# Kernel optimization log

Measured on AMD Instinct MI355X. Metric: run time of the kernel, lower is better.

## Reference

```python
import math
import jax, jax.numpy as jnp
import numpy as np

jax.config.update("jax_enable_x64", True)  # original module computes attention in float64

MIN_NORM = 1e-08
B, S, G = 2, 2048, 16
D_MODEL, NHEAD = 512, 8
KDIM, VDIM = 512, 512
EK, EV = KDIM // NHEAD, VDIM // NHEAD
PARAM_SCALE = 0.02  # keep exp() in range; torch.randn params at this width would overflow exp


def setup_inputs() -> dict:
    key = jax.random.key(0)
    ks = jax.random.split(key, 9)
    f32 = jnp.float32
    return {
        "query": jax.random.normal(ks[0], (B, S, D_MODEL), f32),
        "key": jax.random.normal(ks[1], (B, S, D_MODEL), f32),
        "value": jax.random.normal(ks[2], (B, S, D_MODEL), f32),
        "context": jax.random.normal(ks[3], (B, G, D_MODEL), f32),
        "query_proj": jax.random.normal(ks[4], (1, D_MODEL, KDIM), f32) * PARAM_SCALE,
        "key_proj": jax.random.normal(ks[5], (1, D_MODEL, KDIM), f32) * PARAM_SCALE,
        "value_proj": jax.random.normal(ks[6], (1, D_MODEL, VDIM), f32) * PARAM_SCALE,
        "output_proj": jax.random.normal(ks[7], (1, VDIM, D_MODEL), f32) * PARAM_SCALE,
        "context_proj": jax.random.normal(ks[8], (1, D_MODEL, KDIM), f32) * PARAM_SCALE,
    }


def _causal_attention(queries, keys, values_list):
    # queries: (B,H,G,Ek) context heads; keys: (B,H,S,Ek); values: (B,H,S,Ev)
    q = queries.astype(jnp.float64)
    k = keys.astype(jnp.float64)
    d = k.shape[-1]
    w = jnp.einsum("bhge,bhse->bhgs", q, k) / math.sqrt(d)
    w = jnp.exp(w - jnp.mean(w))            # global mean, as in original
    norms = jnp.cumsum(w, axis=-1)          # (B,H,G,S)
    norms = jnp.where(norms <= MIN_NORM, MIN_NORM, norms)
    out = []
    for v in values_list:
        v = v.astype(jnp.float64)
        # (B,H,G,S,Ev) broadcast outer product, then causal prefix-sum over S
        wv = w[..., None] * v[..., None, :, :]
        rm = jnp.cumsum(wv, axis=-2) / norms[..., None]
        out.append(jnp.swapaxes(rm, -3, -2).astype(jnp.float32))  # (B,H,S,G,Ev)
    return out


def _forward(query, key, value, context, query_proj, key_proj, value_proj, output_proj, context_proj):
    Bb, L, E = query.shape
    Gg = context.shape[1]
    H, Ek, Ev = NHEAD, KDIM // NHEAD, VDIM // NHEAD
    cs = jnp.swapaxes((context @ context_proj).reshape(Bb, Gg, H, Ek), 1, 2)  # (B,H,G,Ek)
    qs = jnp.swapaxes((query @ query_proj).reshape(Bb, L, H, Ek), 1, 2)      # (B,H,S,Ek)
    kk = jnp.swapaxes((key @ key_proj).reshape(Bb, L, H, Ek), 1, 2)          # (B,H,S,Ek)
    vs = jnp.swapaxes((value @ value_proj).reshape(Bb, L, H, Ev), 1, 2)      # (B,H,S,Ev)
    rvm, rkm = _causal_attention(cs, kk, [vs, kk])  # (B,H,S,G,Ev), (B,H,S,G,Ek)
    weights = jnp.einsum("bhse,bhsge->bhsg", qs, rkm)
    weights = jax.nn.softmax(weights, axis=-1)
    out = jnp.einsum("bhsg,bhsge->bhse", weights, rvm)      # (B,H,S,Ev)
    out = jnp.swapaxes(out, 1, 2).reshape(Bb, L, H * Ev)    # (B,S,vdim)
    return out @ output_proj                                 # (B,S,d_model)


def reference(query, key, value, context, query_proj, key_proj, value_proj, output_proj, context_proj):
    return _forward(query, key, value, context, query_proj, key_proj, value_proj, output_proj, context_proj)
```

## Files before the change

### kernel.cpp

```cpp
#include <hip/hip_runtime.h>
#include <hip/hip_bf16.h>

#define BB 2
#define SS 2048
#define GG 16
#define HH 8
#define EE 64
#define DD 512
#define NCHUNK 32
#define CLEN 64
#define CS_STRIDE 132

typedef __attribute__((ext_vector_type(8))) short bf16x8;
typedef __attribute__((ext_vector_type(4))) float f32x4;

static __device__ __forceinline__ short f2bf(float x) {
  union { float f; unsigned u; } v; v.f = x;
  unsigned r = v.u + 0x7fffu + ((v.u >> 16) & 1u);
  return (short)(r >> 16);
}
static __device__ __forceinline__ float bf2f(short s) {
  return __uint_as_float(((unsigned)(unsigned short)s) << 16);
}
static __device__ __forceinline__ void bsplit(float x, short& hi, short& lo) {
  hi = f2bf(x);
  lo = f2bf(x - bf2f(hi));
}

__global__ __launch_bounds__(256) void cvtT4_bf16(const float* __restrict__ w0,
                                                  const float* __restrict__ w1,
                                                  const float* __restrict__ w2,
                                                  const float* __restrict__ w3,
                                                  short* __restrict__ o0,
                                                  short* __restrict__ o1,
                                                  short* __restrict__ o2,
                                                  short* __restrict__ o3) {
  const float* W; short* O;
  if (blockIdx.z == 0)      { W = w0; O = o0; }
  else if (blockIdx.z == 1) { W = w1; O = o1; }
  else if (blockIdx.z == 2) { W = w2; O = o2; }
  else                      { W = w3; O = o3; }
  __shared__ float t[32][33];
  const int tx = threadIdx.x, ty = threadIdx.y;
  const int k0 = blockIdx.x * 32, n0 = blockIdx.y * 32;
#pragma unroll
  for (int i = 0; i < 4; ++i)
    t[ty + i * 8][tx] = W[(size_t)(k0 + ty + i * 8) * DD + n0 + tx];
  __syncthreads();
#pragma unroll
  for (int i = 0; i < 4; ++i)
    O[(size_t)(n0 + ty + i * 8) * DD + k0 + tx] = f2bf(t[tx][ty + i * 8]);
}

#define LDA 72
__global__ __launch_bounds__(256) void proj_gemm(const float* __restrict__ a0,
                                                 const float* __restrict__ a1,
                                                 const float* __restrict__ a2,
                                                 const short* __restrict__ b0,
                                                 const short* __restrict__ b1,
                                                 const short* __restrict__ b2,
                                                 float* __restrict__ c0,
                                                 float* __restrict__ c1,
                                                 float* __restrict__ c2) {
  const float* A; const short* Bt; float* C;
  if (blockIdx.z == 0)      { A = a0; Bt = b0; C = c0; }
  else if (blockIdx.z == 1) { A = a1; Bt = b1; C = c1; }
  else                      { A = a2; Bt = b2; C = c2; }
  const int N = DD, K = DD;
  __shared__ short As[128 * LDA];
  __shared__ short Bs[64 * LDA];
  const int tid = threadIdx.x;
  const int m0 = blockIdx.y * 128, n0 = blockIdx.x * 64;
  const int wv = tid >> 6, lane = tid & 63;
  const int wm = wv * 32;
  const int r = lane & 15, q = lane >> 4;
  f32x4 acc[2][4] = {};
  for (int k0 = 0; k0 < K; k0 += 64) {
    float4 af[4][2];
    bf16x8 bvv[2];
#pragma unroll
    for (int it = 0; it < 4; ++it) {
      int idx = tid + it * 256;
      int row = idx >> 3, colq = (idx & 7) * 8;
      af[it][0] = *(const float4*)(A + (size_t)(m0 + row) * K + k0 + colq);
      af[it][1] = *(const float4*)(A + (size_t)(m0 + row) * K + k0 + colq + 4);
    }
#pragma unroll
    for (int it = 0; it < 2; ++it) {
      int idx = tid + it * 256;
      int row = idx >> 3, colq = (idx & 7) * 8;
      bvv[it] = *(const bf16x8*)(Bt + (size_t)(n0 + row) * K + k0 + colq);
    }
    __syncthreads();
#pragma unroll
    for (int it = 0; it < 4; ++it) {
      int idx = tid + it * 256;
      int row = idx >> 3, colq = (idx & 7) * 8;
      bf16x8 av;
      const float* p0 = (const float*)&af[it][0];
      const float* p1 = (const float*)&af[it][1];
      av[0] = f2bf(p0[0]); av[1] = f2bf(p0[1]); av[2] = f2bf(p0[2]); av[3] = f2bf(p0[3]);
      av[4] = f2bf(p1[0]); av[5] = f2bf(p1[1]); av[6] = f2bf(p1[2]); av[7] = f2bf(p1[3]);
      *(bf16x8*)(&As[row * LDA + colq]) = av;
    }
#pragma unroll
    for (int it = 0; it < 2; ++it) {
      int idx = tid + it * 256;
      int row = idx >> 3, colq = (idx & 7) * 8;
      *(bf16x8*)(&Bs[row * LDA + colq]) = bvv[it];
    }
    __syncthreads();
#pragma unroll
    for (int ks = 0; ks < 2; ++ks) {
      bf16x8 a0r = *(const bf16x8*)(&As[(wm + r) * LDA + ks * 32 + q * 8]);
      bf16x8 a1r = *(const bf16x8*)(&As[(wm + 16 + r) * LDA + ks * 32 + q * 8]);
#pragma unroll
      for (int j = 0; j < 4; ++j) {
        bf16x8 br = *(const bf16x8*)(&Bs[(j * 16 + r) * LDA + ks * 32 + q * 8]);
        acc[0][j] = __builtin_amdgcn_mfma_f32_16x16x32_bf16(a0r, br, acc[0][j], 0, 0, 0);
        acc[1][j] = __builtin_amdgcn_mfma_f32_16x16x32_bf16(a1r, br, acc[1][j], 0, 0, 0);
      }
    }
  }
#pragma unroll
  for (int i = 0; i < 2; ++i)
#pragma unroll
    for (int j = 0; j < 4; ++j)
#pragma unroll
      for (int reg = 0; reg < 4; ++reg) {
        int m = m0 + wm + i * 16 + q * 4 + reg;
        int n = n0 + j * 16 + r;
        C[(size_t)m * N + n] = acc[i][j][reg];
      }
}

__global__ __launch_bounds__(256) void gemm_bf16(const short* __restrict__ A,
                                                 const short* __restrict__ Bt,
                                                 float* __restrict__ C,
                                                 int M, int N, int K) {
  __shared__ short As[128 * LDA];
  __shared__ short Bs[64 * LDA];
  const int tid = threadIdx.x;
  const int m0 = blockIdx.y * 128, n0 = blockIdx.x * 64;
  const int wv = tid >> 6, lane = tid & 63;
  const int wm = wv * 32;
  const int r = lane & 15, q = lane >> 4;
  f32x4 acc[2][4] = {};
  for (int k0 = 0; k0 < K; k0 += 64) {
    bf16x8 av[4], bvv[2];
#pragma unroll
    for (int it = 0; it < 4; ++it) {
      int idx = tid + it * 256;
      int row = idx >> 3, colq = (idx & 7) * 8;
      av[it] = *(const bf16x8*)(A + (size_t)(m0 + row) * K + k0 + colq);
    }
#pragma unroll
    for (int it = 0; it < 2; ++it) {
      int idx = tid + it * 256;
      int row = idx >> 3, colq = (idx & 7) * 8;
      bvv[it] = *(const bf16x8*)(Bt + (size_t)(n0 + row) * K + k0 + colq);
    }
    __syncthreads();
#pragma unroll
    for (int it = 0; it < 4; ++it) {
      int idx = tid + it * 256;
      int row = idx >> 3, colq = (idx & 7) * 8;
      *(bf16x8*)(&As[row * LDA + colq]) = av[it];
    }
#pragma unroll
    for (int it = 0; it < 2; ++it) {
      int idx = tid + it * 256;
      int row = idx >> 3, colq = (idx & 7) * 8;
      *(bf16x8*)(&Bs[row * LDA + colq]) = bvv[it];
    }
    __syncthreads();
#pragma unroll
    for (int ks = 0; ks < 2; ++ks) {
      bf16x8 a0r = *(const bf16x8*)(&As[(wm + r) * LDA + ks * 32 + q * 8]);
      bf16x8 a1r = *(const bf16x8*)(&As[(wm + 16 + r) * LDA + ks * 32 + q * 8]);
#pragma unroll
      for (int j = 0; j < 4; ++j) {
        bf16x8 br = *(const bf16x8*)(&Bs[(j * 16 + r) * LDA + ks * 32 + q * 8]);
        acc[0][j] = __builtin_amdgcn_mfma_f32_16x16x32_bf16(a0r, br, acc[0][j], 0, 0, 0);
        acc[1][j] = __builtin_amdgcn_mfma_f32_16x16x32_bf16(a1r, br, acc[1][j], 0, 0, 0);
      }
    }
  }
#pragma unroll
  for (int i = 0; i < 2; ++i)
#pragma unroll
    for (int j = 0; j < 4; ++j)
#pragma unroll
      for (int reg = 0; reg < 4; ++reg) {
        int m = m0 + wm + i * 16 + q * 4 + reg;
        int n = n0 + j * 16 + r;
        C[(size_t)m * N + n] = acc[i][j][reg];
      }
}

__global__ __launch_bounds__(256) void ctx_gemm(const float* __restrict__ A,
                                                const float* __restrict__ Wm,
                                                float* __restrict__ part) {
  const int nt = blockIdx.x;
  const int ky = blockIdx.y;
  const int tid = threadIdx.x;
  __shared__ float As[32][68];
  __shared__ float Ws[64][68];
  {
    int m = tid >> 3, kq = (tid & 7) * 8;
    float4 a0 = *(const float4*)(A + (size_t)m * DD + ky * 64 + kq);
    float4 a1 = *(const float4*)(A + (size_t)m * DD + ky * 64 + kq + 4);
    As[m][kq + 0] = a0.x; As[m][kq + 1] = a0.y; As[m][kq + 2] = a0.z; As[m][kq + 3] = a0.w;
    As[m][kq + 4] = a1.x; As[m][kq + 5] = a1.y; As[m][kq + 6] = a1.z; As[m][kq + 7] = a1.w;
  }
  {
    int k = tid >> 2, nq = (tid & 3) * 16;
#pragma unroll
    for (int i = 0; i < 4; ++i) {
      float4 wv = *(const float4*)(Wm + (size_t)(ky * 64 + k) * DD + nt * 64 + nq + i * 4);
      Ws[k][nq + i * 4 + 0] = wv.x; Ws[k][nq + i * 4 + 1] = wv.y;
      Ws[k][nq + i * 4 + 2] = wv.z; Ws[k][nq + i * 4 + 3] = wv.w;
    }
  }
  __syncthreads();
  const int tx = tid & 63, my = tid >> 6;
  float acc[8] = {};
  for (int k = 0; k < 64; ++k) {
    float wv = Ws[k][tx];
#pragma unroll
    for (int m = 0; m < 8; ++m) acc[m] += As[my * 8 + m][k] * wv;
  }
#pragma unroll
  for (int m = 0; m < 8; ++m)
    part[((size_t)ky * 32 + my * 8 + m) * DD + nt * 64 + tx] = acc[m];
}

__global__ __launch_bounds__(256) void ctx_reduce(const float* __restrict__ part,
                                                  float* __restrict__ cs) {
  int i = blockIdx.x * 256 + threadIdx.x;
  float s = 0.f;
#pragma unroll
  for (int ky = 0; ky < 8; ++ky) s += part[(size_t)ky * 32 * DD + i];
  cs[i] = s;
}

__global__ __launch_bounds__(256) void scores_kernel(const float* __restrict__ kk,
                                                     const float* __restrict__ cs,
                                                     float* __restrict__ wout) {
  const int bh = blockIdx.y;
  const int b = bh >> 3, h = bh & 7;
  const int s0 = blockIdx.x * 128;
  const int tid = threadIdx.x;
  __shared__ float csL[16][64];
  __shared__ float kkL[128][65];
#pragma unroll
  for (int it = 0; it < 4; ++it) {
    int idx = tid + it * 256;
    int g = idx >> 6, e = idx & 63;
    csL[g][e] = cs[((size_t)(b * GG + g)) * DD + h * EE + e];
  }
  for (int it = 0; it < 32; ++it) {
    int idx = tid + it * 256;
    int s = idx >> 6, e = idx & 63;
    kkL[s][e] = kk[((size_t)(b * SS + s0 + s)) * DD + h * EE + e];
  }
  __syncthreads();
#pragma unroll
  for (int i = 0; i < 8; ++i) {
    int o = i * 256 + tid;
    int g = o >> 7, s = o & 127;
    float d = 0.f;
#pragma unroll
    for (int e = 0; e < 64; ++e) d += csL[g][e] * kkL[s][e];
    wout[((size_t)(bh * GG + g)) * SS + s0 + s] = expf(d * 0.125f);
  }
}

__global__ __launch_bounds__(256) void scanA_kernel(const float* __restrict__ w,
                                                    const float* __restrict__ kk,
                                                    const float* __restrict__ vs,
                                                    float* __restrict__ csums) {
  const int bh = blockIdx.y, c = blockIdx.x;
  const int b = bh >> 3, h = bh & 7;
  const int tid = threadIdx.x;
  const int g = tid >> 4, j = tid & 15;
  __shared__ float wL[16][64];
#pragma unroll
  for (int it = 0; it < 4; ++it) {
    int idx = tid + it * 256;
    int gg = idx >> 6, t = idx & 63;
    wL[gg][t] = w[((size_t)(bh * GG + gg)) * SS + c * CLEN + t];
  }
  __syncthreads();
  float sk0 = 0, sk1 = 0, sk2 = 0, sk3 = 0;
  float sv0 = 0, sv1 = 0, sv2 = 0, sv3 = 0;
  float n = 0;
  for (int t = 0; t < CLEN; ++t) {
    float wg = wL[g][t];
    size_t base = ((size_t)(b * SS + c * CLEN + t)) * DD + h * EE + j * 4;
    float4 k4 = *(const float4*)(kk + base);
    float4 v4 = *(const float4*)(vs + base);
    sk0 += wg * k4.x; sk1 += wg * k4.y; sk2 += wg * k4.z; sk3 += wg * k4.w;
    sv0 += wg * v4.x; sv1 += wg * v4.y; sv2 += wg * v4.z; sv3 += wg * v4.w;
    n += wg;
  }
  size_t ob = ((size_t)((bh * NCHUNK + c) * GG + g)) * CS_STRIDE;
  *(float4*)(csums + ob + j * 4) = make_float4(sk0, sk1, sk2, sk3);
  *(float4*)(csums + ob + 64 + j * 4) = make_float4(sv0, sv1, sv2, sv3);
  if (j == 0) csums[ob + 128] = n;
}

#define LDW 72
#define LDN 40
__global__ __launch_bounds__(256) void chunk_kernel(const float* __restrict__ w,
                                                    const float* __restrict__ kk,
                                                    const float* __restrict__ vs,
                                                    const float* __restrict__ qs,
                                                    const float* __restrict__ csums,
                                                    short* __restrict__ attnbf) {
  const int c = blockIdx.x, bh = blockIdx.y;
  const int b = bh >> 3, h = bh & 7;
  const int tid = threadIdx.x;
  const int lane = tid & 63, wvid = tid >> 6;
  const int r = lane & 15, q = lane >> 4;
  const int sw = wvid * 16;

  __shared__ short qh[64 * LDW], qlo[64 * LDW], khb[64 * LDW], dh[64 * LDW];
  __shared__ short whb[16 * LDW], wlb[16 * LDW], skph[16 * LDW], skpl[16 * LDW];
  __shared__ short svpt[64 * LDN];
  __shared__ float nL[16 * 68];
  __shared__ float npreL[16];
  short* wct = qh;
  short* cmb = qlo;
  short* vt = khb;
  short* uh = dh;

  const int row = tid >> 2, c16 = (tid & 3) * 16;
  const size_t gb = ((size_t)(b * SS + c * CLEN + row)) * DD + h * EE + c16;
  float4 qv[4], kv[4], vv[4];
#pragma unroll
  for (int i = 0; i < 4; ++i) {
    qv[i] = *(const float4*)(qs + gb + i * 4);
    kv[i] = *(const float4*)(kk + gb + i * 4);
    vv[i] = *(const float4*)(vs + gb + i * 4);
  }
  const int g0 = tid >> 4, t4 = (tid & 15) * 4;
  float4 wv4 = *(const float4*)(w + ((size_t)(bh * GG + g0)) * SS + c * CLEN + t4);

  float4 skv = make_float4(0, 0, 0, 0), svv = make_float4(0, 0, 0, 0);
  {
    int c2 = 0;
    for (; c2 + 4 <= c; c2 += 4) {
#pragma unroll
      for (int u = 0; u < 4; ++u) {
        size_t ob2 = ((size_t)((bh * NCHUNK + c2 + u) * GG + g0)) * CS_STRIDE;
        float4 a = *(const float4*)(csums + ob2 + t4);
        float4 bsum = *(const float4*)(csums + ob2 + 64 + t4);
        skv.x += a.x; skv.y += a.y; skv.z += a.z; skv.w += a.w;
        svv.x += bsum.x; svv.y += bsum.y; svv.z += bsum.z; svv.w += bsum.w;
      }
    }
    for (; c2 < c; ++c2) {
      size_t ob2 = ((size_t)((bh * NCHUNK + c2) * GG + g0)) * CS_STRIDE;
      float4 a = *(const float4*)(csums + ob2 + t4);
      float4 bsum = *(const float4*)(csums + ob2 + 64 + t4);
      skv.x += a.x; skv.y += a.y; skv.z += a.z; skv.w += a.w;
      svv.x += bsum.x; svv.y += bsum.y; svv.z += bsum.z; svv.w += bsum.w;
    }
  }
  if (tid < 16) {
    float npr = 0.f;
    for (int c2 = 0; c2 < c; ++c2)
      npr += csums[((size_t)((bh * NCHUNK + c2) * GG + tid)) * CS_STRIDE + 128];
    npreL[tid] = npr;
  }

#pragma unroll
  for (int i = 0; i < 4; ++i) {
    const float* pq = (const float*)&qv[i];
    const float* pk = (const float*)&kv[i];
#pragma unroll
    for (int e = 0; e < 4; ++e) {
      int col = c16 + i * 4 + e;
      short hi, lo;
      bsplit(pq[e], hi, lo);
      qh[row * LDW + col] = hi;
      qlo[row * LDW + col] = lo;
      khb[row * LDW + col] = f2bf(pk[e]);
    }
  }
  {
    const float* pw = (const float*)&wv4;
    const float* ps = (const float*)&skv;
#pragma unroll
    for (int e = 0; e < 4; ++e) {
      short hi, lo;
      bsplit(pw[e], hi, lo);
      whb[g0 * LDW + t4 + e] = hi;
      wlb[g0 * LDW + t4 + e] = lo;
      bsplit(ps[e], hi, lo);
      skph[g0 * LDW + t4 + e] = hi;
      skpl[g0 * LDW + t4 + e] = lo;
    }
  }
  __syncthreads();

#pragma unroll
  for (int gg = 0; gg < 4; ++gg) {
    int g = wvid * 4 + gg;
    float val = bf2f(whb[g * LDW + lane]) + bf2f(wlb[g * LDW + lane]);
#pragma unroll
    for (int d = 1; d < 64; d <<= 1) {
      float tup = __shfl_up(val, d);
      if (lane >= d) val += tup;
    }
    nL[g * 68 + lane] = npreL[g] + val;
  }

  f32x4 accd[4];
  f32x4 accwt = {0.f, 0.f, 0.f, 0.f};
#pragma unroll
  for (int ct = 0; ct < 4; ++ct) accd[ct] = accwt;
#pragma unroll
  for (int kst = 0; kst < 2; ++kst) {
    bf16x8 aq = *(const bf16x8*)(&qh[(sw + r) * LDW + kst * 32 + q * 8]);
    bf16x8 aql = *(const bf16x8*)(&qlo[(sw + r) * LDW + kst * 32 + q * 8]);
    bf16x8 bsh = *(const bf16x8*)(&skph[r * LDW + kst * 32 + q * 8]);
    bf16x8 bsl = *(const bf16x8*)(&skpl[r * LDW + kst * 32 + q * 8]);
    accwt = __builtin_amdgcn_mfma_f32_16x16x32_bf16(aq, bsh, accwt, 0, 0, 0);
    accwt = __builtin_amdgcn_mfma_f32_16x16x32_bf16(aq, bsl, accwt, 0, 0, 0);
    accwt = __builtin_amdgcn_mfma_f32_16x16x32_bf16(aql, bsh, accwt, 0, 0, 0);
#pragma unroll
    for (int ct = 0; ct < 4; ++ct) {
      bf16x8 bk = *(const bf16x8*)(&khb[(ct * 16 + r) * LDW + kst * 32 + q * 8]);
      accd[ct] = __builtin_amdgcn_mfma_f32_16x16x32_bf16(aq, bk, accd[ct], 0, 0, 0);
    }
  }
#pragma unroll
  for (int ct = 0; ct < 4; ++ct)
#pragma unroll
    for (int reg = 0; reg < 4; ++reg) {
      int sl = sw + q * 4 + reg, tl = ct * 16 + r;
      float v = (tl <= sl) ? accd[ct][reg] : 0.f;
      dh[sl * LDW + tl] = f2bf(v);
    }
  __syncthreads();

#pragma unroll
  for (int i = 0; i < 4; ++i) {
    const float* pv = (const float*)&vv[i];
#pragma unroll
    for (int e = 0; e < 4; ++e)
      vt[(c16 + i * 4 + e) * LDW + row] = f2bf(pv[e]);
  }
  {
    const float* pv = (const float*)&svv;
#pragma unroll
    for (int e = 0; e < 4; ++e)
      svpt[(t4 + e) * LDN + g0] = f2bf(pv[e]);
    int ez = tid >> 2, gz = 16 + (tid & 3) * 4;
#pragma unroll
    for (int e = 0; e < 4; ++e) svpt[ez * LDN + gz + e] = 0;
    int tt = tid >> 2, gw = (tid & 3) * 4;
#pragma unroll
    for (int e = 0; e < 4; ++e) {
      wct[tt * LDN + gw + e] = whb[(gw + e) * LDW + tt];
      wct[tt * LDN + 16 + gw + e] = 0;
    }
  }

#pragma unroll
  for (int kst = 0; kst < 2; ++kst) {
    bf16x8 ad = *(const bf16x8*)(&dh[(sw + r) * LDW + kst * 32 + q * 8]);
    bf16x8 bw = *(const bf16x8*)(&whb[r * LDW + kst * 32 + q * 8]);
    bf16x8 bl = *(const bf16x8*)(&wlb[r * LDW + kst * 32 + q * 8]);
    accwt = __builtin_amdgcn_mfma_f32_16x16x32_bf16(ad, bw, accwt, 0, 0, 0);
    accwt = __builtin_amdgcn_mfma_f32_16x16x32_bf16(ad, bl, accwt, 0, 0, 0);
  }
#pragma unroll
  for (int reg = 0; reg < 4; ++reg) {
    int sl = sw + q * 4 + reg;
    float nv = fmaxf(nL[r * 68 + sl], 1e-8f);
    float wt = accwt[reg] / nv;
    float m = wt;
    m = fmaxf(m, __shfl_xor(m, 1));
    m = fmaxf(m, __shfl_xor(m, 2));
    m = fmaxf(m, __shfl_xor(m, 4));
    m = fmaxf(m, __shfl_xor(m, 8));
    float ex = expf(wt - m);
    float den = ex;
    den += __shfl_xor(den, 1);
    den += __shfl_xor(den, 2);
    den += __shfl_xor(den, 4);
    den += __shfl_xor(den, 8);
    float cmv = (ex / den) / nv;
    cmb[sl * LDN + r] = f2bf(cmv);
    cmb[sl * LDN + 16 + r] = 0;
  }
  __syncthreads();

  bf16x8 acm = *(const bf16x8*)(&cmb[(sw + r) * LDN + q * 8]);
  f32x4 accu[4];
#pragma unroll
  for (int ct = 0; ct < 4; ++ct) accu[ct] = (f32x4){0.f, 0.f, 0.f, 0.f};
#pragma unroll
  for (int ct = 0; ct < 4; ++ct) {
    bf16x8 bwc = *(const bf16x8*)(&wct[(ct * 16 + r) * LDN + q * 8]);
    accu[ct] = __builtin_amdgcn_mfma_f32_16x16x32_bf16(acm, bwc, accu[ct], 0, 0, 0);
  }
#pragma unroll
  for (int ct = 0; ct < 4; ++ct)
#pragma unroll
    for (int reg = 0; reg < 4; ++reg) {
      int sl = sw + q * 4 + reg, tl = ct * 16 + r;
      float v = (tl <= sl) ? accu[ct][reg] : 0.f;
      uh[sl * LDW + tl] = f2bf(v);
    }

  f32x4 acco[4];
#pragma unroll
  for (int et = 0; et < 4; ++et) acco[et] = (f32x4){0.f, 0.f, 0.f, 0.f};
#pragma unroll
  for (int et = 0; et < 4; ++et) {
    bf16x8 bs = *(const bf16x8*)(&svpt[(et * 16 + r) * LDN + q * 8]);
    acco[et] = __builtin_amdgcn_mfma_f32_16x16x32_bf16(acm, bs, acco[et], 0, 0, 0);
  }
#pragma unroll
  for (int kst = 0; kst < 2; ++kst) {
    bf16x8 au = *(const bf16x8*)(&uh[(sw + r) * LDW + kst * 32 + q * 8]);
#pragma unroll
    for (int et = 0; et < 4; ++et) {
      bf16x8 bv = *(const bf16x8*)(&vt[(et * 16 + r) * LDW + kst * 32 + q * 8]);
      acco[et] = __builtin_amdgcn_mfma_f32_16x16x32_bf16(au, bv, acco[et], 0, 0, 0);
    }
  }
#pragma unroll
  for (int et = 0; et < 4; ++et)
#pragma unroll
    for (int reg = 0; reg < 4; ++reg) {
      int sl = sw + q * 4 + reg;
      attnbf[((size_t)(b * SS + c * CLEN + sl)) * DD + h * EE + et * 16 + r] =
          f2bf(acco[et][reg]);
    }
}

extern "C" void kernel_launch(void* const* d_in, const int* in_sizes, int n_in,
                              void* d_out, int out_size, void* d_ws, size_t ws_size,
                              hipStream_t stream) {
  const float* query = (const float*)d_in[0];
  const float* key = (const float*)d_in[1];
  const float* value = (const float*)d_in[2];
  const float* context = (const float*)d_in[3];
  const float* query_proj = (const float*)d_in[4];
  const float* key_proj = (const float*)d_in[5];
  const float* value_proj = (const float*)d_in[6];
  const float* output_proj = (const float*)d_in[7];
  const float* context_proj = (const float*)d_in[8];
  float* out = (float*)d_out;

  float* fbase = (float*)d_ws;
  const size_t MS = (size_t)BB * SS * DD;
  float* qs_t = fbase;
  float* kk_t = qs_t + MS;
  float* vs_t = kk_t + MS;
  float* cs_t = vs_t + MS;
  float* wbuf = cs_t + (size_t)BB * GG * DD;
  float* csums = wbuf + (size_t)BB * HH * GG * SS;
  float* part = csums + (size_t)BB * HH * NCHUNK * GG * CS_STRIDE;
  short* Abf = (short*)(part + (size_t)8 * 32 * DD);
  short* Wq = Abf + MS;
  short* Wk = Wq + (size_t)DD * DD;
  short* Wv = Wk + (size_t)DD * DD;
  short* Wo = Wv + (size_t)DD * DD;

  dim3 blk(256);
  dim3 tb(32, 8), tg4(DD / 32, DD / 32, 4);

  cvtT4_bf16<<<tg4, tb, 0, stream>>>(query_proj, key_proj, value_proj, output_proj,
                                     Wq, Wk, Wv, Wo);
  ctx_gemm<<<dim3(8, 8), blk, 0, stream>>>(context, context_proj, part);
  ctx_reduce<<<dim3(BB * GG * DD / 256), blk, 0, stream>>>(part, cs_t);

  proj_gemm<<<dim3(DD / 64, (BB * SS) / 128, 3), blk, 0, stream>>>(
      query, key, value, Wq, Wk, Wv, qs_t, kk_t, vs_t);

  dim3 gsc(SS / 128, BB * HH);
  scores_kernel<<<gsc, blk, 0, stream>>>(kk_t, cs_t, wbuf);

  dim3 gscan(NCHUNK, BB * HH);
  scanA_kernel<<<gscan, blk, 0, stream>>>(wbuf, kk_t, vs_t, csums);
  chunk_kernel<<<gscan, blk, 0, stream>>>(wbuf, kk_t, vs_t, qs_t, csums, Abf);

  gemm_bf16<<<dim3(DD / 64, (BB * SS) / 128), blk, 0, stream>>>(Abf, Wo, out, BB * SS, DD, DD);
}
```

Before: 165.9 us.

## Fuse score computation into scan and chunk kernels using split-bf16 MFMA

Removes the separate scores kernel and its global weight buffer. The exp(cs·k) weights are now recomputed inside both the chunk-sum kernel and the chunk kernel with split-bf16 MFMA (hi/lo products). The per-chunk sums in scanA also move from a scalar FMA loop to MFMA over transposed K and V tiles in shared memory. This saves one launch and a global write/read of the weight tensor, at the cost of duplicated score computation, more shared memory, and bf16 rounding in V/K sums.

```diff
diff --git a/kernel.cpp b/kernel.cpp
--- a/kernel.cpp
+++ b/kernel.cpp
@@ -244,78 +244,138 @@
   cs[i] = s;
 }
 
-__global__ __launch_bounds__(256) void scores_kernel(const float* __restrict__ kk,
-                                                     const float* __restrict__ cs,
-                                                     float* __restrict__ wout) {
-  const int bh = blockIdx.y;
-  const int b = bh >> 3, h = bh & 7;
-  const int s0 = blockIdx.x * 128;
-  const int tid = threadIdx.x;
-  __shared__ float csL[16][64];
-  __shared__ float kkL[128][65];
-#pragma unroll
-  for (int it = 0; it < 4; ++it) {
-    int idx = tid + it * 256;
-    int g = idx >> 6, e = idx & 63;
-    csL[g][e] = cs[((size_t)(b * GG + g)) * DD + h * EE + e];
-  }
-  for (int it = 0; it < 32; ++it) {
-    int idx = tid + it * 256;
-    int s = idx >> 6, e = idx & 63;
-    kkL[s][e] = kk[((size_t)(b * SS + s0 + s)) * DD + h * EE + e];
-  }
-  __syncthreads();
-#pragma unroll
-  for (int i = 0; i < 8; ++i) {
-    int o = i * 256 + tid;
-    int g = o >> 7, s = o & 127;
-    float d = 0.f;
-#pragma unroll
-    for (int e = 0; e < 64; ++e) d += csL[g][e] * kkL[s][e];
-    wout[((size_t)(bh * GG + g)) * SS + s0 + s] = expf(d * 0.125f);
-  }
-}
-
-__global__ __launch_bounds__(256) void scanA_kernel(const float* __restrict__ w,
-                                                    const float* __restrict__ kk,
+#define LDW 72
+#define LDN 40
+
+__global__ __launch_bounds__(256) void scanA_kernel(const float* __restrict__ kk,
                                                     const float* __restrict__ vs,
+                                                    const float* __restrict__ cs,
                                                     float* __restrict__ csums) {
   const int bh = blockIdx.y, c = blockIdx.x;
   const int b = bh >> 3, h = bh & 7;
   const int tid = threadIdx.x;
-  const int g = tid >> 4, j = tid & 15;
-  __shared__ float wL[16][64];
-#pragma unroll
-  for (int it = 0; it < 4; ++it) {
-    int idx = tid + it * 256;
-    int gg = idx >> 6, t = idx & 63;
-    wL[gg][t] = w[((size_t)(bh * GG + gg)) * SS + c * CLEN + t];
-  }
-  __syncthreads();
-  float sk0 = 0, sk1 = 0, sk2 = 0, sk3 = 0;
-  float sv0 = 0, sv1 = 0, sv2 = 0, sv3 = 0;
-  float n = 0;
-  for (int t = 0; t < CLEN; ++t) {
-    float wg = wL[g][t];
-    size_t base = ((size_t)(b * SS + c * CLEN + t)) * DD + h * EE + j * 4;
-    float4 k4 = *(const float4*)(kk + base);
-    float4 v4 = *(const float4*)(vs + base);
-    sk0 += wg * k4.x; sk1 += wg * k4.y; sk2 += wg * k4.z; sk3 += wg * k4.w;
-    sv0 += wg * v4.x; sv1 += wg * v4.y; sv2 += wg * v4.z; sv3 += wg * v4.w;
-    n += wg;
-  }
-  size_t ob = ((size_t)((bh * NCHUNK + c) * GG + g)) * CS_STRIDE;
-  *(float4*)(csums + ob + j * 4) = make_float4(sk0, sk1, sk2, sk3);
-  *(float4*)(csums + ob + 64 + j * 4) = make_float4(sv0, sv1, sv2, sv3);
-  if (j == 0) csums[ob + 128] = n;
-}
-
-#define LDW 72
-#define LDN 40
-__global__ __launch_bounds__(256) void chunk_kernel(const float* __restrict__ w,
-                                                    const float* __restrict__ kk,
+  const int lane = tid & 63, wvid = tid >> 6;
+  const int r = lane & 15, q = lane >> 4;
+
+  __shared__ short csh[16 * LDW], csl[16 * LDW];
+  __shared__ short kh[64 * LDW], kl[64 * LDW];
+  __shared__ short kTh[64 * LDW], kTl[64 * LDW];
+  __shared__ short vT[64 * LDW];
+  __shared__ short wh[16 * LDW], wl[16 * LDW];
+  __shared__ float nPart[4][16];
+
+  const int row = tid >> 2, c16 = (tid & 3) * 16;
+  const size_t gb = ((size_t)(b * SS + c * CLEN + row)) * DD + h * EE + c16;
+  float4 kv[4], vv[4];
+#pragma unroll
+  for (int i = 0; i < 4; ++i) {
+    kv[i] = *(const float4*)(kk + gb + i * 4);
+    vv[i] = *(const float4*)(vs + gb + i * 4);
+  }
+  short hiA[16], loA[16];
+#pragma unroll
+  for (int i = 0; i < 4; ++i) {
+    const float* pk = (const float*)&kv[i];
+#pragma unroll
+    for (int e = 0; e < 4; ++e) bsplit(pk[e], hiA[i * 4 + e], loA[i * 4 + e]);
+  }
+  {
+    bf16x8 p0, p1, p2, p3;
+#pragma unroll
+    for (int e = 0; e < 8; ++e) { p0[e] = hiA[e]; p1[e] = hiA[8 + e]; p2[e] = loA[e]; p3[e] = loA[8 + e]; }
+    *(bf16x8*)(&kh[row * LDW + c16]) = p0;
+    *(bf16x8*)(&kh[row * LDW + c16 + 8]) = p1;
+    *(bf16x8*)(&kl[row * LDW + c16]) = p2;
+    *(bf16x8*)(&kl[row * LDW + c16 + 8]) = p3;
+  }
+#pragma unroll
+  for (int t = 0; t < 16; ++t) {
+    kTh[(c16 + t) * LDW + row] = hiA[t];
+    kTl[(c16 + t) * LDW + row] = loA[t];
+  }
+#pragma unroll
+  for (int i = 0; i < 4; ++i) {
+    const float* pv = (const float*)&vv[i];
+#pragma unroll
+    for (int e = 0; e < 4; ++e) vT[(c16 + i * 4 + e) * LDW + row] = f2bf(pv[e]);
+  }
+  {
+    const int g0 = tid >> 4, t4 = (tid & 15) * 4;
+    float4 csv = *(const float4*)(cs + ((size_t)(b * GG + g0)) * DD + h * EE + t4);
+    const float* pc = (const float*)&csv;
+#pragma unroll
+    for (int e = 0; e < 4; ++e) {
+      short hi, lo;
+      bsplit(pc[e], hi, lo);
+      csh[g0 * LDW + t4 + e] = hi;
+      csl[g0 * LDW + t4 + e] = lo;
+    }
+  }
+  __syncthreads();
+
+  f32x4 accw = {0.f, 0.f, 0.f, 0.f};
+#pragma unroll
+  for (int ks = 0; ks < 2; ++ks) {
+    bf16x8 ah = *(const bf16x8*)(&csh[r * LDW + ks * 32 + q * 8]);
+    bf16x8 al = *(const bf16x8*)(&csl[r * LDW + ks * 32 + q * 8]);
+    bf16x8 bh = *(const bf16x8*)(&kh[(wvid * 16 + r) * LDW + ks * 32 + q * 8]);
+    bf16x8 bl = *(const bf16x8*)(&kl[(wvid * 16 + r) * LDW + ks * 32 + q * 8]);
+    accw = __builtin_amdgcn_mfma_f32_16x16x32_bf16(ah, bh, accw, 0, 0, 0);
+    accw = __builtin_amdgcn_mfma_f32_16x16x32_bf16(ah, bl, accw, 0, 0, 0);
+    accw = __builtin_amdgcn_mfma_f32_16x16x32_bf16(al, bh, accw, 0, 0, 0);
+  }
+  float wf[4];
+#pragma unroll
+  for (int reg = 0; reg < 4; ++reg) {
+    wf[reg] = expf(accw[reg] * 0.125f);
+    short hi, lo;
+    bsplit(wf[reg], hi, lo);
+    int g = q * 4 + reg, t = wvid * 16 + r;
+    wh[g * LDW + t] = hi;
+    wl[g * LDW + t] = lo;
+  }
+#pragma unroll
+  for (int reg = 0; reg < 4; ++reg) {
+    float np = wf[reg];
+    np += __shfl_xor(np, 1);
+    np += __shfl_xor(np, 2);
+    np += __shfl_xor(np, 4);
+    np += __shfl_xor(np, 8);
+    if (r == 0) nPart[wvid][q * 4 + reg] = np;
+  }
+  __syncthreads();
+
+  f32x4 ask = {0.f, 0.f, 0.f, 0.f}, asv = ask;
+#pragma unroll
+  for (int ks = 0; ks < 2; ++ks) {
+    bf16x8 awh = *(const bf16x8*)(&wh[r * LDW + ks * 32 + q * 8]);
+    bf16x8 awl = *(const bf16x8*)(&wl[r * LDW + ks * 32 + q * 8]);
+    bf16x8 bkh = *(const bf16x8*)(&kTh[(wvid * 16 + r) * LDW + ks * 32 + q * 8]);
+    bf16x8 bkl = *(const bf16x8*)(&kTl[(wvid * 16 + r) * LDW + ks * 32 + q * 8]);
+    bf16x8 bv = *(const bf16x8*)(&vT[(wvid * 16 + r) * LDW + ks * 32 + q * 8]);
+    ask = __builtin_amdgcn_mfma_f32_16x16x32_bf16(awh, bkh, ask, 0, 0, 0);
+    ask = __builtin_amdgcn_mfma_f32_16x16x32_bf16(awh, bkl, ask, 0, 0, 0);
+    ask = __builtin_amdgcn_mfma_f32_16x16x32_bf16(awl, bkh, ask, 0, 0, 0);
+    asv = __builtin_amdgcn_mfma_f32_16x16x32_bf16(awh, bv, asv, 0, 0, 0);
+    asv = __builtin_amdgcn_mfma_f32_16x16x32_bf16(awl, bv, asv, 0, 0, 0);
+  }
+#pragma unroll
+  for (int reg = 0; reg < 4; ++reg) {
+    int g = q * 4 + reg, e = wvid * 16 + r;
+    size_t ob = ((size_t)((bh * NCHUNK + c) * GG + g)) * CS_STRIDE;
+    csums[ob + e] = ask[reg];
+    csums[ob + 64 + e] = asv[reg];
+  }
+  if (tid < 16) {
+    size_t ob = ((size_t)((bh * NCHUNK + c) * GG + tid)) * CS_STRIDE;
+    csums[ob + 128] = nPart[0][tid] + nPart[1][tid] + nPart[2][tid] + nPart[3][tid];
+  }
+}
+
+__global__ __launch_bounds__(256) void chunk_kernel(const float* __restrict__ kk,
                                                     const float* __restrict__ vs,
                                                     const float* __restrict__ qs,
+                                                    const float* __restrict__ cs,
                                                     const float* __restrict__ csums,
                                                     short* __restrict__ attnbf) {
   const int c = blockIdx.x, bh = blockIdx.y;
@@ -325,8 +385,9 @@
   const int r = lane & 15, q = lane >> 4;
   const int sw = wvid * 16;
 
-  __shared__ short qh[64 * LDW], qlo[64 * LDW], khb[64 * LDW], dh[64 * LDW];
+  __shared__ short qh[64 * LDW], qlo[64 * LDW], khb[64 * LDW], klo[64 * LDW], dh[64 * LDW];
   __shared__ short whb[16 * LDW], wlb[16 * LDW], skph[16 * LDW], skpl[16 * LDW];
+  __shared__ short cshb[16 * LDW], cslb[16 * LDW];
   __shared__ short svpt[64 * LDN];
   __shared__ float nL[16 * 68];
   __shared__ float npreL[16];
@@ -345,7 +406,7 @@
     vv[i] = *(const float4*)(vs + gb + i * 4);
   }
   const int g0 = tid >> 4, t4 = (tid & 15) * 4;
-  float4 wv4 = *(const float4*)(w + ((size_t)(bh * GG + g0)) * SS + c * CLEN + t4);
+  float4 csv = *(const float4*)(cs + ((size_t)(b * GG + g0)) * DD + h * EE + t4);
 
   float4 skv = make_float4(0, 0, 0, 0), svv = make_float4(0, 0, 0, 0);
   {
@@ -386,21 +447,47 @@
       bsplit(pq[e], hi, lo);
       qh[row * LDW + col] = hi;
       qlo[row * LDW + col] = lo;
-      khb[row * LDW + col] = f2bf(pk[e]);
-    }
-  }
-  {
-    const float* pw = (const float*)&wv4;
+      bsplit(pk[e], hi, lo);
+      khb[row * LDW + col] = hi;
+      klo[row * LDW + col] = lo;
+    }
+  }
+  {
+    const float* pc = (const float*)&csv;
     const float* ps = (const float*)&skv;
 #pragma unroll
     for (int e = 0; e < 4; ++e) {
       short hi, lo;
-      bsplit(pw[e], hi, lo);
-      whb[g0 * LDW + t4 + e] = hi;
-      wlb[g0 * LDW + t4 + e] = lo;
+      bsplit(pc[e], hi, lo);
+      cshb[g0 * LDW + t4 + e] = hi;
+      cslb[g0 * LDW + t4 + e] = lo;
       bsplit(ps[e], hi, lo);
       skph[g0 * LDW + t4 + e] = hi;
       skpl[g0 * LDW + t4 + e] = lo;
+    }
+  }
+  __syncthreads();
+
+  {
+    f32x4 accw = {0.f, 0.f, 0.f, 0.f};
+#pragma unroll
+    for (int ks = 0; ks < 2; ++ks) {
+      bf16x8 ah = *(const bf16x8*)(&cshb[r * LDW + ks * 32 + q * 8]);
+      bf16x8 al = *(const bf16x8*)(&cslb[r * LDW + ks * 32 + q * 8]);
+      bf16x8 bh = *(const bf16x8*)(&khb[(sw + r) * LDW + ks * 32 + q * 8]);
+      bf16x8 bl = *(const bf16x8*)(&klo[(sw + r) * LDW + ks * 32 + q * 8]);
+      accw = __builtin_amdgcn_mfma_f32_16x16x32_bf16(ah, bh, accw, 0, 0, 0);
+      accw = __builtin_amdgcn_mfma_f32_16x16x32_bf16(ah, bl, accw, 0, 0, 0);
+      accw = __builtin_amdgcn_mfma_f32_16x16x32_bf16(al, bh, accw, 0, 0, 0);
+    }
+#pragma unroll
+    for (int reg = 0; reg < 4; ++reg) {
+      float wv = expf(accw[reg] * 0.125f);
+      short hi, lo;
+      bsplit(wv, hi, lo);
+      int g = q * 4 + reg, t = sw + r;
+      whb[g * LDW + t] = hi;
+      wlb[g * LDW + t] = lo;
     }
   }
   __syncthreads();
@@ -564,8 +651,7 @@
   float* kk_t = qs_t + MS;
   float* vs_t = kk_t + MS;
   float* cs_t = vs_t + MS;
-  float* wbuf = cs_t + (size_t)BB * GG * DD;
-  float* csums = wbuf + (size_t)BB * HH * GG * SS;
+  float* csums = cs_t + (size_t)BB * GG * DD;
   float* part = csums + (size_t)BB * HH * NCHUNK * GG * CS_STRIDE;
   short* Abf = (short*)(part + (size_t)8 * 32 * DD);
   short* Wq = Abf + MS;
@@ -584,12 +670,9 @@
   proj_gemm<<<dim3(DD / 64, (BB * SS) / 128, 3), blk, 0, stream>>>(
       query, key, value, Wq, Wk, Wv, qs_t, kk_t, vs_t);
 
-  dim3 gsc(SS / 128, BB * HH);
-  scores_kernel<<<gsc, blk, 0, stream>>>(kk_t, cs_t, wbuf);
-
   dim3 gscan(NCHUNK, BB * HH);
-  scanA_kernel<<<gscan, blk, 0, stream>>>(wbuf, kk_t, vs_t, csums);
-  chunk_kernel<<<gscan, blk, 0, stream>>>(wbuf, kk_t, vs_t, qs_t, csums, Abf);
+  scanA_kernel<<<gscan, blk, 0, stream>>>(kk_t, vs_t, cs_t, csums);
+  chunk_kernel<<<gscan, blk, 0, stream>>>(kk_t, vs_t, qs_t, cs_t, csums, Abf);
 
   gemm_bf16<<<dim3(DD / 64, (BB * SS) / 128), blk, 0, stream>>>(Abf, Wo, out, BB * SS, DD, DD);
 }
```

After: 157.4 us. 1.05x faster.
